# Optimization experiments

Measured on AMD Instinct MI355X. Metric: run time of the kernel, lower is better.

Reference implementation:

```python
import jax, jax.numpy as jnp
import numpy as np

T_WIN, B, N_NODES, D_IN = 3, 1, 50000, 128
E_PER_T = 100000
HID, N_HEADS = 128, 8
D_K = HID // N_HEADS
SQRT_DK = float(np.sqrt(D_K))


def setup_inputs() -> dict:
    key = jax.random.key(0)
    ks = jax.random.split(key, 8)
    w_scale = 0.05
    return {
        "x": jax.random.normal(ks[0], (T_WIN, B, N_NODES, D_IN), jnp.float32),
        "edge_index": jax.random.randint(ks[1], (T_WIN, 2, E_PER_T), 0, N_NODES, jnp.int32),
        "Wq": jax.random.normal(ks[2], (D_IN, HID), jnp.float32) * w_scale,
        "bq": jnp.zeros((HID,), jnp.float32),
        "Wk": jax.random.normal(ks[3], (D_IN, HID), jnp.float32) * w_scale,
        "bk": jnp.zeros((HID,), jnp.float32),
        "Wv": jax.random.normal(ks[4], (D_IN, HID), jnp.float32) * w_scale,
        "bv": jnp.zeros((HID,), jnp.float32),
        "ln_scale": jnp.ones((HID,), jnp.float32),
        "ln_bias": jnp.zeros((HID,), jnp.float32),
        "W1": jax.random.normal(ks[5], (HID, 2 * HID), jnp.float32) * w_scale,
        "b1": jnp.zeros((2 * HID,), jnp.float32),
        "W2": jax.random.normal(ks[6], (2 * HID, HID), jnp.float32) * w_scale,
        "b2": jnp.zeros((HID,), jnp.float32),
    }


def _segment_softmax(a, seg, n):
    # a: [E, B, H], seg: [E] target node ids -> softmax per target node
    m = jax.ops.segment_max(a, seg, num_segments=n)           # [N, B, H]
    ex = jnp.exp(a - m[seg])
    s = jax.ops.segment_sum(ex, seg, num_segments=n)          # [N, B, H]
    return ex / (s[seg] + 1e-16)


def _ffn(h, ln_scale, ln_bias, W1, b1, W2, b2):
    # LayerNorm -> Linear -> GELU -> Linear, residual add (norm=True, skip=False, dropout=0)
    mu = jnp.mean(h, axis=-1, keepdims=True)
    var = jnp.mean((h - mu) ** 2, axis=-1, keepdims=True)
    hn = (h - mu) / jnp.sqrt(var + 1e-5) * ln_scale + ln_bias
    r = jax.nn.gelu(hn @ W1 + b1, approximate=False) @ W2 + b2
    return h + r


def reference(x, edge_index, Wq, bq, Wk, bk, Wv, bv, ln_scale, ln_bias, W1, b1, W2, b2):
    T, Bd, N, D = x.shape
    # per-node QKV once per time step (use_RTE=False): [T, B, N, HID]
    q_all = jnp.einsum("tbnd,dh->tbnh", x, Wq) + bq
    k_all = jnp.einsum("tbnd,dh->tbnh", x, Wk) + bk
    v_all = jnp.einsum("tbnd,dh->tbnh", x, Wv) + bv

    xs, cs, ss = [], [], []
    for t_tar in range(T):
        atts, msgs, segs = [], [], []
        for t_src in range(t_tar + 1):
            src = edge_index[t_src, 0]
            tar = edge_index[t_src, 1]
            # gather edge endpoints, edge axis leading: [E, B, H, D_K]
            q_e = jnp.take(q_all[t_tar], tar, axis=1).swapaxes(0, 1).reshape(-1, Bd, N_HEADS, D_K)
            k_e = jnp.take(k_all[t_src], src, axis=1).swapaxes(0, 1).reshape(-1, Bd, N_HEADS, D_K)
            v_e = jnp.take(v_all[t_src], src, axis=1).swapaxes(0, 1).reshape(-1, Bd, N_HEADS, D_K)
            atts.append(jnp.sum(q_e * k_e, axis=-1) / SQRT_DK)  # [E, B, H]
            msgs.append(v_e)
            segs.append(tar)
        att = jnp.concatenate(atts, axis=0)   # [Etot, B, H]
        msg = jnp.concatenate(msgs, axis=0)   # [Etot, B, H, D_K]
        seg = jnp.concatenate(segs, axis=0)   # [Etot]
        Et = att.shape[0]

        p_c = _segment_softmax(att, seg, N)
        p_s = _segment_softmax(-att, seg, N)
        res = (msg * p_c[..., None]).reshape(Et, Bd, HID)
        spu = (msg * p_s[..., None]).reshape(Et, Bd, HID)
        causal_hat = jax.ops.segment_sum(res, seg, num_segments=N).swapaxes(0, 1)    # [B, N, HID]
        spurious_hat = jax.ops.segment_sum(spu, seg, num_segments=N).swapaxes(0, 1)  # [B, N, HID]

        causal = _ffn(causal_hat + x[t_tar], ln_scale, ln_bias, W1, b1, W2, b2)
        spurious = _ffn(spurious_hat, ln_scale, ln_bias, W1, b1, W2, b2)
        xs.append(causal + spurious)
        cs.append(causal)
        ss.append(spurious)

    # pack (xs, cs, ss) as one array: [3, T, B, N, HID]
    return jnp.stack([jnp.stack(xs), jnp.stack(cs), jnp.stack(ss)])
```

## Files before the change

kernel.cpp:

```cpp
#include <hip/hip_runtime.h>
#include <math.h>

#define T_WIN   3
#define N_NODES 50000
#define HID     128
#define E_PER_T 100000
#define NH      8
#define DK      16
#define CAP     64


typedef unsigned short u16;
typedef __attribute__((ext_vector_type(8))) short bf16x8;
typedef __attribute__((ext_vector_type(4))) float f32x4;

__device__ __forceinline__ u16 f2bf(float v) {
    unsigned u = __float_as_uint(v);
    return (u16)((u + 0x7fffu + ((u >> 16) & 1u)) >> 16);
}
__device__ __forceinline__ float bf2f(u16 u) {
    return __uint_as_float(((unsigned)u) << 16);
}
__device__ __forceinline__ f32x4 mfma16(bf16x8 a, bf16x8 b, f32x4 c) {
    return __builtin_amdgcn_mfma_f32_16x16x32_bf16(a, b, c, 0, 0, 0);
}

__global__ __launch_bounds__(256) void wsplit_kernel(
    const float* __restrict__ src, u16* __restrict__ hi, u16* __restrict__ lo,
    int R, int C)
{
    int i = blockIdx.x * 256 + threadIdx.x;
    if (i >= R * C) return;
    int r = i / C, c = i - r * C;
    float v = src[i];
    u16 h = f2bf(v);
    hi[c * R + r] = h;
    lo[c * R + r] = f2bf(v - bf2f(h));
}

__global__ __launch_bounds__(256) void wt_kernel(
    const float* __restrict__ src, u16* __restrict__ dst, int R, int C)
{
    int i = blockIdx.x * 256 + threadIdx.x;
    if (i >= R * C) return;
    int r = i / C, c = i - r * C;
    dst[c * R + r] = f2bf(src[i]);
}

__global__ __launch_bounds__(256) void zero_counts_kernel(int* cursor)
{
    int i = blockIdx.x * 256 + threadIdx.x;
    if (i < T_WIN * N_NODES) cursor[i] = 0;
}

__global__ __launch_bounds__(256) void hist_kernel(
    const int* __restrict__ ei, int* counts)
{
    int i = blockIdx.x * 256 + threadIdx.x;
    if (i >= T_WIN * E_PER_T) return;
    int ts = i / E_PER_T;
    int e  = i - ts * E_PER_T;
    int tar = ei[(ts * 2 + 1) * E_PER_T + e];
    atomicAdd(&counts[ts * N_NODES + tar], 1);
}

__global__ __launch_bounds__(1024) void scan_kernel(
    const int* __restrict__ counts, int* __restrict__ offs)
{
    __shared__ int buf[1024];
    __shared__ int carry;
    const int ts = blockIdx.x;
    const int tid = threadIdx.x;
    if (tid == 0) carry = 0;
    __syncthreads();
    for (int base = 0; base < N_NODES; base += 1024) {
        int i = base + tid;
        int v = (i < N_NODES) ? counts[ts * N_NODES + i] : 0;
        buf[tid] = v;
        __syncthreads();
        for (int o = 1; o < 1024; o <<= 1) {
            int t = (tid >= o) ? buf[tid - o] : 0;
            __syncthreads();
            buf[tid] += t;
            __syncthreads();
        }
        int incl = buf[tid];
        if (i < N_NODES) offs[ts * (N_NODES + 1) + i] = carry + incl - v;
        __syncthreads();
        if (tid == 1023) carry += incl;
        __syncthreads();
    }
    if (tid == 0) offs[ts * (N_NODES + 1) + N_NODES] = carry;
}

__global__ __launch_bounds__(256) void copy_cursor_kernel(
    const int* __restrict__ offs, int* cursor)
{
    int i = blockIdx.x * 256 + threadIdx.x;
    if (i >= T_WIN * N_NODES) return;
    int ts = i / N_NODES;
    int n  = i - ts * N_NODES;
    cursor[i] = offs[ts * (N_NODES + 1) + n];
}

__global__ __launch_bounds__(256) void fill_kernel(
    const int* __restrict__ ei, int* cursor, int* __restrict__ srcbuf)
{
    int i = blockIdx.x * 256 + threadIdx.x;
    if (i >= T_WIN * E_PER_T) return;
    int ts = i / E_PER_T;
    int e  = i - ts * E_PER_T;
    int src = ei[(ts * 2) * E_PER_T + e];
    int tar = ei[(ts * 2 + 1) * E_PER_T + e];
    int pos = atomicAdd(&cursor[ts * N_NODES + tar], 1);
    srcbuf[ts * E_PER_T + pos] = src;
}

__global__ __launch_bounds__(256) void project_all_kernel(
    const float* __restrict__ x,
    const u16* __restrict__ QTh, const u16* __restrict__ QTl, const float* __restrict__ bq,
    const u16* __restrict__ KTh, const u16* __restrict__ KTl, const float* __restrict__ bk,
    const u16* __restrict__ VTh, const u16* __restrict__ VTl, const float* __restrict__ bv,
    u16* __restrict__ Qall, u16* __restrict__ Kall, u16* __restrict__ Vall)
{
    const int p  = blockIdx.y;
    const int ts = p / 3, mat = p - ts * 3;
    const u16 *WTh, *WTl; const float* b; u16* O;
    if (mat == 0)      { WTh = QTh; WTl = QTl; b = bq; O = Qall; }
    else if (mat == 1) { WTh = KTh; WTl = KTl; b = bk; O = Kall; }
    else               { WTh = VTh; WTl = VTl; b = bv; O = Vall; }
    const size_t NHID = (size_t)N_NODES * HID;
    const float* __restrict__ xs = x + (size_t)ts * NHID;
    O += (size_t)ts * NHID;

    __shared__ u16 xhS[64 * 128];
    __shared__ u16 xlS[64 * 128];
    const int tid = threadIdx.x;
    const int n0 = blockIdx.x * 64;

    {
        const int row = tid >> 2, q = tid & 3;
        const int n = n0 + row;
        const float4* xp = (const float4*)(xs + (size_t)n * 128 + q * 32);
        const int sbase = row * 128;
#pragma unroll
        for (int i = 0; i < 4; ++i) {
            float4 a = make_float4(0.f, 0.f, 0.f, 0.f), c = a;
            if (n < N_NODES) { a = xp[2 * i]; c = xp[2 * i + 1]; }
            float vv[8] = {a.x, a.y, a.z, a.w, c.x, c.y, c.z, c.w};
            uint4 uh, ul;
            unsigned* ph = (unsigned*)&uh;
            unsigned* pl = (unsigned*)&ul;
#pragma unroll
            for (int j = 0; j < 4; ++j) {
                u16 h0 = f2bf(vv[2 * j]), h1 = f2bf(vv[2 * j + 1]);
                ph[j] = (unsigned)h0 | ((unsigned)h1 << 16);
                u16 l0 = f2bf(vv[2 * j] - bf2f(h0));
                u16 l1 = f2bf(vv[2 * j + 1] - bf2f(h1));
                pl[j] = (unsigned)l0 | ((unsigned)l1 << 16);
            }
            int ch = (q * 4 + i) ^ (row & 15);
            *(uint4*)&xhS[sbase + ch * 8] = uh;
            *(uint4*)&xlS[sbase + ch * 8] = ul;
        }
    }
    __syncthreads();

    const int lane = tid & 63, w = tid >> 6;
    const int l15 = lane & 15, l4 = lane >> 4;
    f32x4 acc[4][2];
    const f32x4 z4 = {0.f, 0.f, 0.f, 0.f};
#pragma unroll
    for (int m = 0; m < 4; ++m)
#pragma unroll
        for (int n = 0; n < 2; ++n) acc[m][n] = z4;

#pragma unroll
    for (int ks = 0; ks < 4; ++ks) {
        const int ch = (ks * 4 + l4) ^ l15;
        bf16x8 ah[4], al[4];
#pragma unroll
        for (int m = 0; m < 4; ++m) {
            ah[m] = *(const bf16x8*)&xhS[(m * 16 + l15) * 128 + ch * 8];
            al[m] = *(const bf16x8*)&xlS[(m * 16 + l15) * 128 + ch * 8];
        }
        bf16x8 bh[2], bl[2];
#pragma unroll
        for (int n = 0; n < 2; ++n) {
            size_t wo = (size_t)(w * 32 + n * 16 + l15) * 128 + ks * 32 + l4 * 8;
            bh[n] = *(const bf16x8*)(WTh + wo);
            bl[n] = *(const bf16x8*)(WTl + wo);
        }
#pragma unroll
        for (int m = 0; m < 4; ++m)
#pragma unroll
            for (int n = 0; n < 2; ++n) {
                acc[m][n] = mfma16(ah[m], bh[n], acc[m][n]);
                acc[m][n] = mfma16(ah[m], bl[n], acc[m][n]);
                acc[m][n] = mfma16(al[m], bh[n], acc[m][n]);
            }
    }

#pragma unroll
    for (int n = 0; n < 2; ++n) {
        int c = w * 32 + n * 16 + l15;
        float bb = b[c];
#pragma unroll
        for (int m = 0; m < 4; ++m)
#pragma unroll
            for (int j = 0; j < 4; ++j) {
                int r = m * 16 + l4 * 4 + j;
                int ng = n0 + r;
                if (ng < N_NODES)
                    O[(size_t)ng * 128 + c] = f2bf(acc[m][n][j] + bb);
            }
    }
}

__global__ __launch_bounds__(256) void attn_fused_kernel(
    const u16* __restrict__ Qall, const u16* __restrict__ Kall,
    const u16* __restrict__ Vall,
    const int* __restrict__ offs, const int* __restrict__ srcbuf,
    float* __restrict__ hat_c, float* __restrict__ hat_s, int t_tar)
{
    __shared__ float logitS[4][CAP][NH];
    __shared__ int   srcS[4][CAP];
    const int lane = threadIdx.x & 63;
    const int wave = threadIdx.x >> 6;
    const int node = blockIdx.x * 4 + wave;
    if (node >= N_NODES) return;

    const size_t NHID = (size_t)N_NODES * HID;
    const u16* __restrict__ Qt = Qall + (size_t)t_tar * NHID;
    const int h  = lane & 7;
    const int j8 = lane >> 3;

    float (*lg)[NH] = logitS[wave];
    int* sx = srcS[wave];

    uint4 q0, q1;
    {
        const uint4* qp = (const uint4*)(Qt + (size_t)node * HID + h * DK);
        q0 = qp[0]; q1 = qp[1];
    }

    float mx = -1e30f, mn = 1e30f;
    int base = 0;
    for (int ts = 0; ts <= t_tar; ++ts) {
        const int beg = offs[ts * (N_NODES + 1) + node];
        const int end = offs[ts * (N_NODES + 1) + node + 1];
        const u16* __restrict__ K = Kall + (size_t)ts * NHID;
        const int* __restrict__ sb = srcbuf + (size_t)ts * E_PER_T;
        for (int j = beg + j8; j < end; j += 8) {
            int idx = base + (j - beg);
            int src = sb[j];
            const uint4* kp = (const uint4*)(K + (size_t)src * HID + h * DK);
            uint4 k0 = kp[0], k1 = kp[1];
            float s = 0.f;
            const unsigned* pa = (const unsigned*)&q0;
            const unsigned* pb = (const unsigned*)&k0;
#pragma unroll
            for (int i = 0; i < 4; ++i)
                s += __uint_as_float(pa[i] << 16) * __uint_as_float(pb[i] << 16)
                   + __uint_as_float(pa[i] & 0xffff0000u) * __uint_as_float(pb[i] & 0xffff0000u);
            pa = (const unsigned*)&q1; pb = (const unsigned*)&k1;
#pragma unroll
            for (int i = 0; i < 4; ++i)
                s += __uint_as_float(pa[i] << 16) * __uint_as_float(pb[i] << 16)
                   + __uint_as_float(pa[i] & 0xffff0000u) * __uint_as_float(pb[i] & 0xffff0000u);
            s *= 0.25f;
            mx = fmaxf(mx, s);
            mn = fminf(mn, s);
            if (idx < CAP) { lg[idx][h] = s; if (h == 0) sx[idx] = src; }
        }
        base += end - beg;
    }
    const int dtot = base;
    if (dtot == 0) {
        size_t bidx = (size_t)node * HID + 2 * lane;
        *(float2*)(hat_c + bidx) = make_float2(0.f, 0.f);
        *(float2*)(hat_s + bidx) = make_float2(0.f, 0.f);
        return;
    }
#pragma unroll
    for (int o = 8; o < 64; o <<= 1) {
        mx = fmaxf(mx, __shfl_xor(mx, o));
        mn = fminf(mn, __shfl_xor(mn, o));
    }

    float sc = 0.f, ss = 0.f;
    {
        const int nfast = dtot < CAP ? dtot : CAP;
        for (int idx = j8; idx < nfast; idx += 8) {
            float a = lg[idx][h];
            sc += __expf(a - mx);
            ss += __expf(mn - a);
        }
        if (dtot > CAP) {
            int b2 = 0;
            for (int ts = 0; ts <= t_tar; ++ts) {
                const int beg = offs[ts * (N_NODES + 1) + node];
                const int end = offs[ts * (N_NODES + 1) + node + 1];
                const u16* K = Kall + (size_t)ts * NHID;
                const int* sb = srcbuf + (size_t)ts * E_PER_T;
                for (int j = beg + j8; j < end; j += 8) {
                    int idx = b2 + (j - beg);
                    if (idx >= CAP) {
                        int src = sb[j];
                        const uint4* kp = (const uint4*)(K + (size_t)src * HID + h * DK);
                        uint4 k0 = kp[0], k1 = kp[1];
                        float s = 0.f;
                        const unsigned* pa = (const unsigned*)&q0;
                        const unsigned* pb = (const unsigned*)&k0;
#pragma unroll
                        for (int i = 0; i < 4; ++i)
                            s += __uint_as_float(pa[i] << 16) * __uint_as_float(pb[i] << 16)
                               + __uint_as_float(pa[i] & 0xffff0000u) * __uint_as_float(pb[i] & 0xffff0000u);
                        pa = (const unsigned*)&q1; pb = (const unsigned*)&k1;
#pragma unroll
                        for (int i = 0; i < 4; ++i)
                            s += __uint_as_float(pa[i] << 16) * __uint_as_float(pb[i] << 16)
                               + __uint_as_float(pa[i] & 0xffff0000u) * __uint_as_float(pb[i] & 0xffff0000u);
                        s *= 0.25f;
                        sc += __expf(s - mx);
                        ss += __expf(mn - s);
                    }
                }
                b2 += end - beg;
            }
        }
    }
#pragma unroll
    for (int o = 8; o < 64; o <<= 1) {
        sc += __shfl_xor(sc, o);
        ss += __shfl_xor(ss, o);
    }

    const int h2 = lane >> 3;
    const float mc   = __shfl(mx, h2);
    const float mnn  = __shfl(mn, h2);
    const float isc  = 1.f / (__shfl(sc, h2) + 1e-16f);
    const float iss  = 1.f / (__shfl(ss, h2) + 1e-16f);

    float aC0 = 0.f, aC1 = 0.f, aS0 = 0.f, aS1 = 0.f;
    base = 0;
    for (int ts = 0; ts <= t_tar; ++ts) {
        const int beg = offs[ts * (N_NODES + 1) + node];
        const int end = offs[ts * (N_NODES + 1) + node + 1];
        const u16* __restrict__ V = Vall + (size_t)ts * NHID;
        const int* __restrict__ sb = srcbuf + (size_t)ts * E_PER_T;
        for (int j = beg; j < end; ++j) {
            int idx = base + (j - beg);
            float a; int src;
            if (idx < CAP) {
                a = lg[idx][h2];
                src = sx[idx];
            } else {
                src = sb[j];
                unsigned qd = *(const unsigned*)(Qt + (size_t)node * HID + 2 * lane);
                unsigned kd = *(const unsigned*)(Kall + (size_t)ts * NHID + (size_t)src * HID + 2 * lane);
                float p = __uint_as_float(qd << 16) * __uint_as_float(kd << 16)
                        + __uint_as_float(qd & 0xffff0000u) * __uint_as_float(kd & 0xffff0000u);
                p += __shfl_xor(p, 1);
                p += __shfl_xor(p, 2);
                p += __shfl_xor(p, 4);
                a = p * 0.25f;
            }
            float pc = __expf(a - mc) * isc;
            float ps = __expf(mnn - a) * iss;
            unsigned v2 = *(const unsigned*)(V + (size_t)src * HID + 2 * lane);
            float v0 = __uint_as_float(v2 << 16);
            float v1 = __uint_as_float(v2 & 0xffff0000u);
            aC0 += v0 * pc; aC1 += v1 * pc;
            aS0 += v0 * ps; aS1 += v1 * ps;
        }
        base += end - beg;
    }
    size_t bidx = (size_t)node * HID + 2 * lane;
    *(float2*)(hat_c + bidx) = make_float2(aC0, aC1);
    *(float2*)(hat_s + bidx) = make_float2(aS0, aS1);
}

__global__ __launch_bounds__(256, 3) void ffn_out_kernel(
    const float* __restrict__ hat_c, const float* __restrict__ hat_s,
    const float* __restrict__ x,
    const float* __restrict__ ln_s, const float* __restrict__ ln_b,
    const u16* __restrict__ W1T, const float* __restrict__ b1,
    const u16* __restrict__ W2T, const float* __restrict__ b2,
    float* __restrict__ out, int t_tar)
{
    __shared__ u16 hnS[2][32 * 128];
    __shared__ u16 hidS[2][32 * 256];
    const int n0 = blockIdx.x * 32;
    const int tid = threadIdx.x;
    const float* __restrict__ xt = x + (size_t)t_tar * N_NODES * 128;
    const size_t TS = (size_t)T_WIN * N_NODES * HID;
    const size_t outbase = (size_t)t_tar * N_NODES * HID;

    const int lane = tid & 63;
    const int wave = tid >> 6;
    const int br   = wave >> 1;
    const int wv   = wave & 1;
    const int l15 = lane & 15, l4 = lane >> 4;
    const f32x4 z4 = {0.f, 0.f, 0.f, 0.f};
    const float* __restrict__ hat = br ? hat_s : hat_c;

    {
        const int row = (tid & 127) >> 2, q = tid & 3;
        const int n = n0 + row;
        float v[32];
        float s = 0.f, s2 = 0.f;
        if (n < N_NODES) {
            const float4* hp = (const float4*)(hat + (size_t)n * 128 + q * 32);
            const float4* xp = (const float4*)(xt + (size_t)n * 128 + q * 32);
#pragma unroll
            for (int i = 0; i < 8; ++i) {
                float4 a = hp[i];
                if (br == 0) {
                    float4 bx = xp[i];
                    a.x += bx.x; a.y += bx.y; a.z += bx.z; a.w += bx.w;
                }
                v[4 * i] = a.x; v[4 * i + 1] = a.y;
                v[4 * i + 2] = a.z; v[4 * i + 3] = a.w;
                s  += a.x + a.y + a.z + a.w;
                s2 += a.x * a.x + a.y * a.y + a.z * a.z + a.w * a.w;
            }
        } else {
#pragma unroll
            for (int i = 0; i < 32; ++i) v[i] = 0.f;
        }
        s  += __shfl_xor(s, 1);  s  += __shfl_xor(s, 2);
        s2 += __shfl_xor(s2, 1); s2 += __shfl_xor(s2, 2);
        float mu  = s * (1.f / 128.f);
        float var = s2 * (1.f / 128.f) - mu * mu;
        float rstd = rsqrtf(var + 1e-5f);
        const int sbase = row * 128;
#pragma unroll
        for (int i = 0; i < 4; ++i) {
            uint4 uh; unsigned* ph = (unsigned*)&uh;
#pragma unroll
            for (int j = 0; j < 4; ++j) {
                int c0 = q * 32 + i * 8 + 2 * j;
                float h0 = (v[i * 8 + 2 * j]     - mu) * rstd * ln_s[c0]     + ln_b[c0];
                float h1 = (v[i * 8 + 2 * j + 1] - mu) * rstd * ln_s[c0 + 1] + ln_b[c0 + 1];
                if (n >= N_NODES) { h0 = 0.f; h1 = 0.f; }
                ph[j] = (unsigned)f2bf(h0) | ((unsigned)f2bf(h1) << 16);
            }
            int ch = (q * 4 + i) ^ (row & 15);
            *(uint4*)&hnS[br][sbase + ch * 8] = uh;
        }
    }
    __syncthreads();

    {
        f32x4 a1[2][8];
#pragma unroll
        for (int m = 0; m < 2; ++m)
#pragma unroll
            for (int n = 0; n < 8; ++n) a1[m][n] = z4;

#pragma unroll
        for (int ks = 0; ks < 4; ++ks) {
            const int ch = (ks * 4 + l4) ^ l15;
            bf16x8 af[2];
#pragma unroll
            for (int m = 0; m < 2; ++m)
                af[m] = *(const bf16x8*)&hnS[br][(m * 16 + l15) * 128 + ch * 8];
#pragma unroll
            for (int n = 0; n < 8; ++n) {
                bf16x8 bfr = *(const bf16x8*)(W1T + (size_t)(wv * 128 + n * 16 + l15) * 128
                                                  + ks * 32 + l4 * 8);
#pragma unroll
                for (int m = 0; m < 2; ++m)
                    a1[m][n] = mfma16(af[m], bfr, a1[m][n]);
            }
        }
#pragma unroll
        for (int n = 0; n < 8; ++n) {
            int c = wv * 128 + n * 16 + l15;
            float bb = b1[c];
#pragma unroll
            for (int m = 0; m < 2; ++m)
#pragma unroll
                for (int j = 0; j < 4; ++j) {
                    int r = m * 16 + l4 * 4 + j;
                    float zz = a1[m][n][j] + bb;
                    float g = 0.5f * zz * (1.f + erff(zz * 0.70710678118654752f));
                    hidS[br][r * 256 + (((c >> 3) ^ (r & 15)) * 8) + (c & 7)] = f2bf(g);
                }
        }
    }
    __syncthreads();

    f32x4 a2[2][4];
#pragma unroll
    for (int m = 0; m < 2; ++m)
#pragma unroll
        for (int n = 0; n < 4; ++n) a2[m][n] = z4;

#pragma unroll
    for (int ks = 0; ks < 8; ++ks) {
        const int ch = (ks * 4 + l4) ^ l15;
        bf16x8 af[2];
#pragma unroll
        for (int m = 0; m < 2; ++m)
            af[m] = *(const bf16x8*)&hidS[br][(m * 16 + l15) * 256 + ch * 8];
#pragma unroll
        for (int n = 0; n < 4; ++n) {
            bf16x8 bfr = *(const bf16x8*)(W2T + (size_t)(wv * 64 + n * 16 + l15) * 256
                                              + ks * 32 + l4 * 8);
#pragma unroll
            for (int m = 0; m < 2; ++m)
                a2[m][n] = mfma16(af[m], bfr, a2[m][n]);
        }
    }

    float* sxS = (float*)&hnS[0][0];
    if (br == 1) {
#pragma unroll
        for (int n = 0; n < 4; ++n) {
            int c = wv * 64 + n * 16 + l15;
            float bb = b2[c];
#pragma unroll
            for (int m = 0; m < 2; ++m)
#pragma unroll
                for (int j = 0; j < 4; ++j) {
                    int r = m * 16 + l4 * 4 + j;
                    int ng = n0 + r;
                    float val = a2[m][n][j] + bb;
                    if (ng < N_NODES) {
                        size_t idx = (size_t)ng * 128 + c;
                        val += hat_s[idx];
                        out[2 * TS + outbase + idx] = val;
                    }
                    sxS[r * 128 + c] = val;
                }
        }
    }
    __syncthreads();
    if (br == 0) {
#pragma unroll
        for (int n = 0; n < 4; ++n) {
            int c = wv * 64 + n * 16 + l15;
            float bb = b2[c];
#pragma unroll
            for (int m = 0; m < 2; ++m)
#pragma unroll
                for (int j = 0; j < 4; ++j) {
                    int r = m * 16 + l4 * 4 + j;
                    int ng = n0 + r;
                    if (ng < N_NODES) {
                        size_t idx = (size_t)ng * 128 + c;
                        float val = a2[m][n][j] + bb + hat_c[idx] + xt[idx];
                        float sv = sxS[r * 128 + c];
                        size_t o = outbase + idx;
                        out[o]      = val + sv;
                        out[TS + o] = val;
                    }
                }
        }
    }
}

extern "C" void kernel_launch(void* const* d_in, const int* in_sizes, int n_in,
                              void* d_out, int out_size, void* d_ws, size_t ws_size,
                              hipStream_t stream) {
    const float* x    = (const float*)d_in[0];
    const int*   ei   = (const int*)  d_in[1];
    const float* Wq   = (const float*)d_in[2];
    const float* bq   = (const float*)d_in[3];
    const float* Wk   = (const float*)d_in[4];
    const float* bk   = (const float*)d_in[5];
    const float* Wv   = (const float*)d_in[6];
    const float* bv   = (const float*)d_in[7];
    const float* ln_s = (const float*)d_in[8];
    const float* ln_b = (const float*)d_in[9];
    const float* W1   = (const float*)d_in[10];
    const float* b1   = (const float*)d_in[11];
    const float* W2   = (const float*)d_in[12];
    const float* b2   = (const float*)d_in[13];
    float* out = (float*)d_out;

    const size_t NHID = (size_t)N_NODES * HID;
    char* p = (char*)d_ws;
    auto alloc = [&p](size_t bytes) -> void* {
        void* r = (void*)p;
        p += (bytes + 255) & ~(size_t)255;
        return r;
    };
    float* hat_c = (float*)alloc(NHID * 4);
    float* hat_s = (float*)alloc(NHID * 4);
    int* offs    = (int*)alloc((size_t)T_WIN * (N_NODES + 1) * 4);
    int* cursor  = (int*)alloc((size_t)T_WIN * N_NODES * 4);
    int* srcbuf  = (int*)alloc((size_t)T_WIN * E_PER_T * 4);
    u16* WqTh = (u16*)alloc(128 * 128 * 2);
    u16* WqTl = (u16*)alloc(128 * 128 * 2);
    u16* WkTh = (u16*)alloc(128 * 128 * 2);
    u16* WkTl = (u16*)alloc(128 * 128 * 2);
    u16* WvTh = (u16*)alloc(128 * 128 * 2);
    u16* WvTl = (u16*)alloc(128 * 128 * 2);
    u16* W1T  = (u16*)alloc(128 * 256 * 2);
    u16* W2T  = (u16*)alloc(256 * 128 * 2);
    u16* Qall = (u16*)alloc(3 * NHID * 2);
    u16* Kall = (u16*)alloc(3 * NHID * 2);
    u16* Vall = (u16*)alloc(3 * NHID * 2);

    const int PROJ_BLOCKS = (N_NODES + 63) / 64;
    const int FFN_BLOCKS  = (N_NODES + 31) / 32;
    const int NODE_BLOCKS = (N_NODES + 3) / 4;
    const int TN_BLOCKS   = (T_WIN * N_NODES + 255) / 256;
    const int TE_BLOCKS   = (T_WIN * E_PER_T + 255) / 256;

    wsplit_kernel<<<64, 256, 0, stream>>>(Wq, WqTh, WqTl, 128, 128);
    wsplit_kernel<<<64, 256, 0, stream>>>(Wk, WkTh, WkTl, 128, 128);
    wsplit_kernel<<<64, 256, 0, stream>>>(Wv, WvTh, WvTl, 128, 128);
    wt_kernel<<<128, 256, 0, stream>>>(W1, W1T, 128, 256);
    wt_kernel<<<128, 256, 0, stream>>>(W2, W2T, 256, 128);

    zero_counts_kernel<<<TN_BLOCKS, 256, 0, stream>>>(cursor);
    hist_kernel<<<TE_BLOCKS, 256, 0, stream>>>(ei, cursor);
    scan_kernel<<<T_WIN, 1024, 0, stream>>>(cursor, offs);
    copy_cursor_kernel<<<TN_BLOCKS, 256, 0, stream>>>(offs, cursor);
    fill_kernel<<<TE_BLOCKS, 256, 0, stream>>>(ei, cursor, srcbuf);

    {
        dim3 pg(PROJ_BLOCKS, 9);
        project_all_kernel<<<pg, 256, 0, stream>>>(
            x, WqTh, WqTl, bq, WkTh, WkTl, bk, WvTh, WvTl, bv,
            Qall, Kall, Vall);
    }

    for (int t = 0; t < T_WIN; ++t) {
        attn_fused_kernel<<<NODE_BLOCKS, 256, 0, stream>>>(
            Qall, Kall, Vall, offs, srcbuf, hat_c, hat_s, t);
        ffn_out_kernel<<<FFN_BLOCKS, 256, 0, stream>>>(
            hat_c, hat_s, x, ln_s, ln_b, W1T, b1, W2T, b2, out, t);
    }
}
```

Before: 1.171 ms.

## Batch all timesteps per launch, chunk FFN hidden layer to cut LDS, merge weight prep

Attention and FFN kernels now take the timestep from blockIdx.y, so each runs once over all three timesteps instead of six alternating launches. The hat buffers grow to hold every timestep. The FFN kernel computes the 256-wide hidden layer in four 64-column chunks, double-buffered in shared memory, accumulating into the second GEMM. This shrinks LDS use so the occupancy hint can rise from 3 to 5. The five weight-prep launches become one kernel. The aim is fewer launches and serialization gaps and better FFN occupancy, at the cost of more hat memory and more barriers per FFN block.

```diff
diff --git a/kernel.cpp b/kernel.cpp
--- a/kernel.cpp
+++ b/kernel.cpp
@@ -25,26 +25,36 @@
     return __builtin_amdgcn_mfma_f32_16x16x32_bf16(a, b, c, 0, 0, 0);
 }
 
-__global__ __launch_bounds__(256) void wsplit_kernel(
-    const float* __restrict__ src, u16* __restrict__ hi, u16* __restrict__ lo,
-    int R, int C)
-{
+__global__ __launch_bounds__(256) void wprep_kernel(
+    const float* __restrict__ Wq, const float* __restrict__ Wk,
+    const float* __restrict__ Wv, const float* __restrict__ W1,
+    const float* __restrict__ W2,
+    u16* __restrict__ WqTh, u16* __restrict__ WqTl,
+    u16* __restrict__ WkTh, u16* __restrict__ WkTl,
+    u16* __restrict__ WvTh, u16* __restrict__ WvTl,
+    u16* __restrict__ W1T, u16* __restrict__ W2T)
+{
+    const int y = blockIdx.y;
     int i = blockIdx.x * 256 + threadIdx.x;
-    if (i >= R * C) return;
-    int r = i / C, c = i - r * C;
-    float v = src[i];
-    u16 h = f2bf(v);
-    hi[c * R + r] = h;
-    lo[c * R + r] = f2bf(v - bf2f(h));
-}
-
-__global__ __launch_bounds__(256) void wt_kernel(
-    const float* __restrict__ src, u16* __restrict__ dst, int R, int C)
-{
-    int i = blockIdx.x * 256 + threadIdx.x;
-    if (i >= R * C) return;
-    int r = i / C, c = i - r * C;
-    dst[c * R + r] = f2bf(src[i]);
+    if (y < 3) {
+        if (i >= 128 * 128) return;
+        const float* src = (y == 0) ? Wq : (y == 1) ? Wk : Wv;
+        u16* hi = (y == 0) ? WqTh : (y == 1) ? WkTh : WvTh;
+        u16* lo = (y == 0) ? WqTl : (y == 1) ? WkTl : WvTl;
+        int r = i >> 7, c = i & 127;
+        float v = src[i];
+        u16 h = f2bf(v);
+        hi[c * 128 + r] = h;
+        lo[c * 128 + r] = f2bf(v - bf2f(h));
+    } else if (y == 3) {
+        if (i >= 128 * 256) return;
+        int r = i >> 8, c = i & 255;
+        W1T[c * 128 + r] = f2bf(W1[i]);
+    } else {
+        if (i >= 256 * 128) return;
+        int r = i >> 7, c = i & 127;
+        W2T[c * 256 + r] = f2bf(W2[i]);
+    }
 }
 
 __global__ __launch_bounds__(256) void zero_counts_kernel(int* cursor)
@@ -221,16 +231,19 @@
     const u16* __restrict__ Qall, const u16* __restrict__ Kall,
     const u16* __restrict__ Vall,
     const int* __restrict__ offs, const int* __restrict__ srcbuf,
-    float* __restrict__ hat_c, float* __restrict__ hat_s, int t_tar)
+    float* __restrict__ hat_c_all, float* __restrict__ hat_s_all)
 {
     __shared__ float logitS[4][CAP][NH];
     __shared__ int   srcS[4][CAP];
+    const int t_tar = blockIdx.y;
     const int lane = threadIdx.x & 63;
     const int wave = threadIdx.x >> 6;
     const int node = blockIdx.x * 4 + wave;
     if (node >= N_NODES) return;
 
     const size_t NHID = (size_t)N_NODES * HID;
+    float* __restrict__ hat_c = hat_c_all + (size_t)t_tar * NHID;
+    float* __restrict__ hat_s = hat_s_all + (size_t)t_tar * NHID;
     const u16* __restrict__ Qt = Qall + (size_t)t_tar * NHID;
     const int h  = lane & 7;
     const int j8 = lane >> 3;
@@ -381,21 +394,25 @@
     *(float2*)(hat_s + bidx) = make_float2(aS0, aS1);
 }
 
-__global__ __launch_bounds__(256, 3) void ffn_out_kernel(
-    const float* __restrict__ hat_c, const float* __restrict__ hat_s,
+__global__ __launch_bounds__(256, 5) void ffn_out_kernel(
+    const float* __restrict__ hat_c_all, const float* __restrict__ hat_s_all,
     const float* __restrict__ x,
     const float* __restrict__ ln_s, const float* __restrict__ ln_b,
     const u16* __restrict__ W1T, const float* __restrict__ b1,
     const u16* __restrict__ W2T, const float* __restrict__ b2,
-    float* __restrict__ out, int t_tar)
+    float* __restrict__ out)
 {
     __shared__ u16 hnS[2][32 * 128];
-    __shared__ u16 hidS[2][32 * 256];
+    __shared__ u16 chS[2][2][32 * 64];
+    const int t_tar = blockIdx.y;
     const int n0 = blockIdx.x * 32;
     const int tid = threadIdx.x;
-    const float* __restrict__ xt = x + (size_t)t_tar * N_NODES * 128;
+    const size_t NHID = (size_t)N_NODES * HID;
+    const float* __restrict__ hat_c = hat_c_all + (size_t)t_tar * NHID;
+    const float* __restrict__ hat_s = hat_s_all + (size_t)t_tar * NHID;
+    const float* __restrict__ xt = x + (size_t)t_tar * NHID;
     const size_t TS = (size_t)T_WIN * N_NODES * HID;
-    const size_t outbase = (size_t)t_tar * N_NODES * HID;
+    const size_t outbase = (size_t)t_tar * NHID;
 
     const int lane = tid & 63;
     const int wave = tid >> 6;
@@ -452,13 +469,19 @@
     }
     __syncthreads();
 
-    {
-        f32x4 a1[2][8];
+    f32x4 a2[2][4];
+#pragma unroll
+    for (int m = 0; m < 2; ++m)
+#pragma unroll
+        for (int n = 0; n < 4; ++n) a2[m][n] = z4;
+
+#pragma unroll
+    for (int cc = 0; cc < 4; ++cc) {
+        f32x4 a1[2][2];
 #pragma unroll
         for (int m = 0; m < 2; ++m)
 #pragma unroll
-            for (int n = 0; n < 8; ++n) a1[m][n] = z4;
-
+            for (int n = 0; n < 2; ++n) a1[m][n] = z4;
 #pragma unroll
         for (int ks = 0; ks < 4; ++ks) {
             const int ch = (ks * 4 + l4) ^ l15;
@@ -467,18 +490,19 @@
             for (int m = 0; m < 2; ++m)
                 af[m] = *(const bf16x8*)&hnS[br][(m * 16 + l15) * 128 + ch * 8];
 #pragma unroll
-            for (int n = 0; n < 8; ++n) {
-                bf16x8 bfr = *(const bf16x8*)(W1T + (size_t)(wv * 128 + n * 16 + l15) * 128
-                                                  + ks * 32 + l4 * 8);
+            for (int n = 0; n < 2; ++n) {
+                bf16x8 bfr = *(const bf16x8*)(W1T
+                    + (size_t)(cc * 64 + wv * 32 + n * 16 + l15) * 128 + ks * 32 + l4 * 8);
 #pragma unroll
                 for (int m = 0; m < 2; ++m)
                     a1[m][n] = mfma16(af[m], bfr, a1[m][n]);
             }
         }
-#pragma unroll
-        for (int n = 0; n < 8; ++n) {
-            int c = wv * 128 + n * 16 + l15;
-            float bb = b1[c];
+        u16* chw = &chS[cc & 1][br][0];
+#pragma unroll
+        for (int n = 0; n < 2; ++n) {
+            int cl = wv * 32 + n * 16 + l15;
+            float bb = b1[cc * 64 + cl];
 #pragma unroll
             for (int m = 0; m < 2; ++m)
 #pragma unroll
@@ -486,32 +510,26 @@
                     int r = m * 16 + l4 * 4 + j;
                     float zz = a1[m][n][j] + bb;
                     float g = 0.5f * zz * (1.f + erff(zz * 0.70710678118654752f));
-                    hidS[br][r * 256 + (((c >> 3) ^ (r & 15)) * 8) + (c & 7)] = f2bf(g);
+                    chw[r * 64 + (((cl >> 3) ^ (r & 7)) * 8) + (cl & 7)] = f2bf(g);
                 }
         }
-    }
-    __syncthreads();
-
-    f32x4 a2[2][4];
-#pragma unroll
-    for (int m = 0; m < 2; ++m)
-#pragma unroll
-        for (int n = 0; n < 4; ++n) a2[m][n] = z4;
-
-#pragma unroll
-    for (int ks = 0; ks < 8; ++ks) {
-        const int ch = (ks * 4 + l4) ^ l15;
-        bf16x8 af[2];
-#pragma unroll
-        for (int m = 0; m < 2; ++m)
-            af[m] = *(const bf16x8*)&hidS[br][(m * 16 + l15) * 256 + ch * 8];
-#pragma unroll
-        for (int n = 0; n < 4; ++n) {
-            bf16x8 bfr = *(const bf16x8*)(W2T + (size_t)(wv * 64 + n * 16 + l15) * 256
-                                              + ks * 32 + l4 * 8);
+        __syncthreads();
+        const u16* chr = &chS[cc & 1][br][0];
+#pragma unroll
+        for (int ks2 = 0; ks2 < 2; ++ks2) {
+            const int ch8 = (ks2 * 4 + l4) ^ (l15 & 7);
+            bf16x8 af[2];
 #pragma unroll
             for (int m = 0; m < 2; ++m)
-                a2[m][n] = mfma16(af[m], bfr, a2[m][n]);
+                af[m] = *(const bf16x8*)&chr[(m * 16 + l15) * 64 + ch8 * 8];
+#pragma unroll
+            for (int n = 0; n < 4; ++n) {
+                bf16x8 bfr = *(const bf16x8*)(W2T
+                    + (size_t)(wv * 64 + n * 16 + l15) * 256 + cc * 64 + ks2 * 32 + l4 * 8);
+#pragma unroll
+                for (int m = 0; m < 2; ++m)
+                    a2[m][n] = mfma16(af[m], bfr, a2[m][n]);
+            }
         }
     }
 
@@ -588,8 +606,8 @@
         p += (bytes + 255) & ~(size_t)255;
         return r;
     };
-    float* hat_c = (float*)alloc(NHID * 4);
-    float* hat_s = (float*)alloc(NHID * 4);
+    float* hat_c = (float*)alloc(3 * NHID * 4);
+    float* hat_s = (float*)alloc(3 * NHID * 4);
     int* offs    = (int*)alloc((size_t)T_WIN * (N_NODES + 1) * 4);
     int* cursor  = (int*)alloc((size_t)T_WIN * N_NODES * 4);
     int* srcbuf  = (int*)alloc((size_t)T_WIN * E_PER_T * 4);
@@ -611,11 +629,12 @@
     const int TN_BLOCKS   = (T_WIN * N_NODES + 255) / 256;
     const int TE_BLOCKS   = (T_WIN * E_PER_T + 255) / 256;
 
-    wsplit_kernel<<<64, 256, 0, stream>>>(Wq, WqTh, WqTl, 128, 128);
-    wsplit_kernel<<<64, 256, 0, stream>>>(Wk, WkTh, WkTl, 128, 128);
-    wsplit_kernel<<<64, 256, 0, stream>>>(Wv, WvTh, WvTl, 128, 128);
-    wt_kernel<<<128, 256, 0, stream>>>(W1, W1T, 128, 256);
-    wt_kernel<<<128, 256, 0, stream>>>(W2, W2T, 256, 128);
+    {
+        dim3 wg(128, 5);
+        wprep_kernel<<<wg, 256, 0, stream>>>(
+            Wq, Wk, Wv, W1, W2,
+            WqTh, WqTl, WkTh, WkTl, WvTh, WvTl, W1T, W2T);
+    }
 
     zero_counts_kernel<<<TN_BLOCKS, 256, 0, stream>>>(cursor);
     hist_kernel<<<TE_BLOCKS, 256, 0, stream>>>(ei, cursor);
@@ -630,10 +649,15 @@
             Qall, Kall, Vall);
     }
 
-    for (int t = 0; t < T_WIN; ++t) {
-        attn_fused_kernel<<<NODE_BLOCKS, 256, 0, stream>>>(
-            Qall, Kall, Vall, offs, srcbuf, hat_c, hat_s, t);
-        ffn_out_kernel<<<FFN_BLOCKS, 256, 0, stream>>>(
-            hat_c, hat_s, x, ln_s, ln_b, W1T, b1, W2T, b2, out, t);
-    }
-}
+    {
+        dim3 ag(NODE_BLOCKS, T_WIN);
+        attn_fused_kernel<<<ag, 256, 0, stream>>>(
+            Qall, Kall, Vall, offs, srcbuf, hat_c, hat_s);
+    }
+
+    {
+        dim3 fg(FFN_BLOCKS, T_WIN);
+        ffn_out_kernel<<<fg, 256, 0, stream>>>(
+            hat_c, hat_s, x, ln_s, ln_b, W1T, b1, W2T, b2, out);
+    }
+}
```

Result: faster. 1.119 ms (-4.5%).
